# Kernel tuning notes

Measured on AMD Instinct MI355X. Metric: run time of the kernel, lower is better.

The kernel has to match this reference:

```python
import jax, jax.numpy as jnp
import numpy as np

B, A, H, W, N = 16, 9, 64, 64, 40


def setup_inputs() -> dict:
    key = jax.random.key(0)
    k1, k2, k3, k4, k5, k6 = jax.random.split(key, 6)
    # Anchor shapes (w, h) in pixel units, 9 anchors (3 scales x 3 aspect ratios)
    scales = jnp.array([32.0, 64.0, 128.0], dtype=jnp.float32)
    ratios = jnp.array([0.5, 1.0, 2.0], dtype=jnp.float32)
    ws = (scales[:, None] * jnp.sqrt(ratios)[None, :]).reshape(-1)  # (9,)
    hs = (scales[:, None] / jnp.sqrt(ratios)[None, :]).reshape(-1)
    anc = jnp.stack([ws, hs], axis=-1)  # (A, 2)
    # Grid of cell centers for a 512x512 image with stride 8 -> 64x64 grid
    stride = 8.0
    xs = (jnp.arange(W, dtype=jnp.float32) + 0.5) * stride
    ys = (jnp.arange(H, dtype=jnp.float32) + 0.5) * stride
    gx, gy = jnp.meshgrid(xs, ys, indexing='xy')  # (H, W)
    grid = jnp.broadcast_to(jnp.stack([gx, gy], axis=-1)[None], (B, H, W, 2)).astype(jnp.float32)
    # Predicted offsets: tx, ty in (-0.5, 0.5); tw, th small
    txy = jax.random.uniform(k1, (B, A, H, W, 2), jnp.float32, -0.5, 0.5)
    twh = jax.random.normal(k2, (B, A, H, W, 2), jnp.float32) * 0.2
    offsets = jnp.concatenate([txy, twh], axis=-1)  # (B, A, H, W, 4)
    # Ground-truth boxes (x_tl, y_tl, x_br, y_br, class), well-formed
    img = 512.0
    x1 = jax.random.uniform(k3, (B, N), jnp.float32, 0.0, img - 64.0)
    y1 = jax.random.uniform(k4, (B, N), jnp.float32, 0.0, img - 64.0)
    bw = jax.random.uniform(k5, (B, N), jnp.float32, 8.0, 64.0)
    bh = jax.random.uniform(k6, (B, N), jnp.float32, 8.0, 64.0)
    cls = jnp.zeros((B, N), jnp.float32)
    bboxes = jnp.stack([x1, y1, x1 + bw, y1 + bh, cls], axis=-1)  # (B, N, 5)
    return {"anc": anc, "grid": grid, "offsets": offsets, "bboxes": bboxes}


def reference(anc, grid, offsets, bboxes):
    # --- GenerateAnchor: (B, A, H, W, 4) corner boxes centered on grid ---
    half = (anc * 0.5)[None, :, None, None, :]      # (1, A, 1, 1, 2)
    g = grid[:, None]                               # (B, 1, H, W, 2)
    anchors = jnp.concatenate([g - half, g + half], axis=-1)  # (B, A, H, W, 4)

    # --- GenerateProposal (YOLO): center-shift by txy, scale wh by exp(twh) ---
    cx = (anchors[..., 0] + anchors[..., 2]) * 0.5 + offsets[..., 0]
    cy = (anchors[..., 1] + anchors[..., 3]) * 0.5 + offsets[..., 1]
    pw = (anchors[..., 2] - anchors[..., 0]) * jnp.exp(offsets[..., 2])
    ph = (anchors[..., 3] - anchors[..., 1]) * jnp.exp(offsets[..., 3])
    proposals = jnp.stack([cx - pw * 0.5, cy - ph * 0.5,
                           cx + pw * 0.5, cy + ph * 0.5], axis=-1)  # (B, A, H, W, 4)

    # --- IoU: (B, A*H*W, N) via broadcasting (no explicit repeat) ---
    Bsz = proposals.shape[0]
    p = proposals.reshape(Bsz, -1, 1, 4)   # (B, AHW, 1, 4)
    bb = bboxes[:, None, :, :4]            # (B, 1, N, 4)
    x_tl = jnp.maximum(p[..., 0], bb[..., 0])
    y_tl = jnp.maximum(p[..., 1], bb[..., 1])
    x_br = jnp.minimum(p[..., 2], bb[..., 2])
    y_br = jnp.minimum(p[..., 3], bb[..., 3])
    inter = jnp.clip(x_br - x_tl, 0.0) * jnp.clip(y_br - y_tl, 0.0)
    area_p = (p[..., 2] - p[..., 0]) * (p[..., 3] - p[..., 1])
    area_b = (bb[..., 2] - bb[..., 0]) * (bb[..., 3] - bb[..., 1])
    iou_mat = inter / (area_p + area_b - inter)    # (B, AHW, N)
    return iou_mat
```

## Files before the change

### kernel.cpp

```cpp
#include <hip/hip_runtime.h>

#define BB 16
#define AA 9
#define HH 64
#define WW 64
#define NN 40

constexpr int PPB   = AA * HH * WW;
constexpr int BLOCK = 256;
constexpr int BLOCKS_PER_B = PPB / BLOCK;
constexpr int F4_PER_P     = NN / 4;

typedef float vfloat4 __attribute__((ext_vector_type(4)));

__global__ __launch_bounds__(BLOCK) void iou_kernel(
    const float* __restrict__ anc,
    const float* __restrict__ grid,
    const float* __restrict__ offsets,
    const float* __restrict__ bboxes,
    float* __restrict__ out)
{
    __shared__ float4 sbox[NN];
    __shared__ float4 sp4[BLOCK];

    const int tid = threadIdx.x;
    const int blk = blockIdx.x;
    const int b        = blk / BLOCKS_PER_B;
    const int blk_in_b = blk % BLOCKS_PER_B;

    if (tid < NN) {
        const float* bb = bboxes + (size_t)(b * NN + tid) * 5;
        sbox[tid] = make_float4(bb[0], bb[1], bb[2], bb[3]);
    }

    const int p_in_b = blk_in_b * BLOCK + tid;
    const int a  = p_in_b >> 12;
    const int hw = p_in_b & 4095;
    const int h  = hw >> 6;
    const int w  = hw & 63;

    const float hwid = anc[a * 2 + 0] * 0.5f;
    const float hhgt = anc[a * 2 + 1] * 0.5f;

    const float2 g   = *reinterpret_cast<const float2*>(grid + (size_t)((b * HH + h) * WW + w) * 2);
    const float4 off = *reinterpret_cast<const float4*>(offsets + (size_t)(b * PPB + p_in_b) * 4);

    const float ax1 = g.x - hwid, ax2 = g.x + hwid;
    const float ay1 = g.y - hhgt, ay2 = g.y + hhgt;
    const float cx = (ax1 + ax2) * 0.5f + off.x;
    const float cy = (ay1 + ay2) * 0.5f + off.y;
    const float pw = (ax2 - ax1) * __expf(off.z);
    const float ph = (ay2 - ay1) * __expf(off.w);
    sp4[tid] = make_float4(cx - pw * 0.5f, cy - ph * 0.5f,
                           cx + pw * 0.5f, cy + ph * 0.5f);

    __syncthreads();

    vfloat4* outf4 = reinterpret_cast<vfloat4*>(out) +
                     (size_t)(b * PPB + blk_in_b * BLOCK) * F4_PER_P;

    #pragma unroll
    for (int i = 0; i < F4_PER_P; ++i) {
        const unsigned f = (unsigned)(tid + i * BLOCK);
        const unsigned p = f / 10u;
        const int n0 = (int)(f - p * 10u) * 4;

        const float4 pb = sp4[p];
        const float ap  = (pb.z - pb.x) * (pb.w - pb.y);

        vfloat4 res;
        #pragma unroll
        for (int k = 0; k < 4; ++k) {
            const float4 bb4 = sbox[n0 + k];
            const float ab  = (bb4.z - bb4.x) * (bb4.w - bb4.y);
            const float xtl = fmaxf(pb.x, bb4.x);
            const float ytl = fmaxf(pb.y, bb4.y);
            const float xbr = fminf(pb.z, bb4.z);
            const float ybr = fminf(pb.w, bb4.w);
            const float iw = fmaxf(xbr - xtl, 0.0f);
            const float ih = fmaxf(ybr - ytl, 0.0f);
            const float inter = iw * ih;
            const float den = ap + ab - inter;
            res[k] = inter * __builtin_amdgcn_rcpf(den);
        }
        __builtin_nontemporal_store(res, outf4 + f);
    }
}

extern "C" void kernel_launch(void* const* d_in, const int* in_sizes, int n_in,
                              void* d_out, int out_size, void* d_ws, size_t ws_size,
                              hipStream_t stream) {
    const float* anc     = (const float*)d_in[0];
    const float* grid    = (const float*)d_in[1];
    const float* offsets = (const float*)d_in[2];
    const float* bboxes  = (const float*)d_in[3];
    float* out = (float*)d_out;

    const int nblocks = BB * BLOCKS_PER_B;
    iou_kernel<<<nblocks, BLOCK, 0, stream>>>(anc, grid, offsets, bboxes, out);
}
```

Before: 21.69 us.

## Process two tiles per block with double-buffered shared memory prefetch

```diff
diff --git a/kernel.cpp b/kernel.cpp
--- a/kernel.cpp
+++ b/kernel.cpp
@@ -8,8 +8,11 @@
 
 constexpr int PPB   = AA * HH * WW;
 constexpr int BLOCK = 256;
-constexpr int BLOCKS_PER_B = PPB / BLOCK;
-constexpr int F4_PER_P     = NN / 4;
+constexpr int TPB   = PPB / BLOCK;
+constexpr int TILES = BB * TPB;
+constexpr int TILES_PER_BLOCK = 2;
+constexpr int NBLOCKS = TILES / TILES_PER_BLOCK;
+constexpr int F4_PER_P = NN / 4;
 
 typedef float vfloat4 __attribute__((ext_vector_type(4)));
 
@@ -20,71 +23,88 @@
     const float* __restrict__ bboxes,
     float* __restrict__ out)
 {
-    __shared__ float4 sbox[NN];
-    __shared__ float4 sp4[BLOCK];
+    __shared__ float4 sbox[2][NN];
+    __shared__ float4 sp4[2][BLOCK];
 
     const int tid = threadIdx.x;
-    const int blk = blockIdx.x;
-    const int b        = blk / BLOCKS_PER_B;
-    const int blk_in_b = blk % BLOCKS_PER_B;
 
-    if (tid < NN) {
-        const float* bb = bboxes + (size_t)(b * NN + tid) * 5;
-        sbox[tid] = make_float4(bb[0], bb[1], bb[2], bb[3]);
-    }
+    float2 g;  float4 off;  float hwid, hhgt;  float4 box;
 
-    const int p_in_b = blk_in_b * BLOCK + tid;
-    const int a  = p_in_b >> 12;
-    const int hw = p_in_b & 4095;
-    const int h  = hw >> 6;
-    const int w  = hw & 63;
+    auto load_tile = [&](int t) {
+        const int b  = t / TPB;
+        const int tb = t - b * TPB;
+        const int p  = tb * BLOCK + tid;
+        const int a  = p >> 12;
+        const int hw = p & 4095;
+        const int h  = hw >> 6;
+        const int w  = hw & 63;
+        hwid = anc[a * 2 + 0] * 0.5f;
+        hhgt = anc[a * 2 + 1] * 0.5f;
+        g   = *reinterpret_cast<const float2*>(grid + (size_t)((b * HH + h) * WW + w) * 2);
+        off = *reinterpret_cast<const float4*>(offsets + ((size_t)b * PPB + p) * 4);
+        if (tid < NN) {
+            const float* bb = bboxes + (size_t)(b * NN + tid) * 5;
+            box = make_float4(bb[0], bb[1], bb[2], bb[3]);
+        }
+    };
 
-    const float hwid = anc[a * 2 + 0] * 0.5f;
-    const float hhgt = anc[a * 2 + 1] * 0.5f;
+    auto decode_tile = [&](int buf) {
+        const float ax1 = g.x - hwid, ax2 = g.x + hwid;
+        const float ay1 = g.y - hhgt, ay2 = g.y + hhgt;
+        const float cx = (ax1 + ax2) * 0.5f + off.x;
+        const float cy = (ay1 + ay2) * 0.5f + off.y;
+        const float pw = (ax2 - ax1) * __expf(off.z);
+        const float ph = (ay2 - ay1) * __expf(off.w);
+        sp4[buf][tid] = make_float4(cx - pw * 0.5f, cy - ph * 0.5f,
+                                    cx + pw * 0.5f, cy + ph * 0.5f);
+        if (tid < NN) sbox[buf][tid] = box;
+    };
 
-    const float2 g   = *reinterpret_cast<const float2*>(grid + (size_t)((b * HH + h) * WW + w) * 2);
-    const float4 off = *reinterpret_cast<const float4*>(offsets + (size_t)(b * PPB + p_in_b) * 4);
+    auto store_tile = [&](int t, int buf) {
+        const int b  = t / TPB;
+        const int tb = t - b * TPB;
+        vfloat4* outf4 = reinterpret_cast<vfloat4*>(out) +
+                         ((size_t)b * PPB + (size_t)tb * BLOCK) * F4_PER_P;
+        #pragma unroll
+        for (int i = 0; i < F4_PER_P; ++i) {
+            const unsigned f = (unsigned)(tid + i * BLOCK);
+            const unsigned p = f / 10u;
+            const int n0 = (int)(f - p * 10u) * 4;
 
-    const float ax1 = g.x - hwid, ax2 = g.x + hwid;
-    const float ay1 = g.y - hhgt, ay2 = g.y + hhgt;
-    const float cx = (ax1 + ax2) * 0.5f + off.x;
-    const float cy = (ay1 + ay2) * 0.5f + off.y;
-    const float pw = (ax2 - ax1) * __expf(off.z);
-    const float ph = (ay2 - ay1) * __expf(off.w);
-    sp4[tid] = make_float4(cx - pw * 0.5f, cy - ph * 0.5f,
-                           cx + pw * 0.5f, cy + ph * 0.5f);
+            const float4 pb = sp4[buf][p];
+            const float ap  = (pb.z - pb.x) * (pb.w - pb.y);
 
+            vfloat4 res;
+            #pragma unroll
+            for (int k = 0; k < 4; ++k) {
+                const float4 bb4 = sbox[buf][n0 + k];
+                const float ab  = (bb4.z - bb4.x) * (bb4.w - bb4.y);
+                const float xtl = fmaxf(pb.x, bb4.x);
+                const float ytl = fmaxf(pb.y, bb4.y);
+                const float xbr = fminf(pb.z, bb4.z);
+                const float ybr = fminf(pb.w, bb4.w);
+                const float iw = fmaxf(xbr - xtl, 0.0f);
+                const float ih = fmaxf(ybr - ytl, 0.0f);
+                const float inter = iw * ih;
+                const float den = ap + ab - inter;
+                res[k] = inter * __builtin_amdgcn_rcpf(den);
+            }
+            __builtin_nontemporal_store(res, outf4 + f);
+        }
+    };
+
+    const int t0 = blockIdx.x * TILES_PER_BLOCK;
+
+    load_tile(t0);
+    decode_tile(0);
     __syncthreads();
 
-    vfloat4* outf4 = reinterpret_cast<vfloat4*>(out) +
-                     (size_t)(b * PPB + blk_in_b * BLOCK) * F4_PER_P;
+    load_tile(t0 + 1);
+    store_tile(t0, 0);
 
-    #pragma unroll
-    for (int i = 0; i < F4_PER_P; ++i) {
-        const unsigned f = (unsigned)(tid + i * BLOCK);
-        const unsigned p = f / 10u;
-        const int n0 = (int)(f - p * 10u) * 4;
-
-        const float4 pb = sp4[p];
-        const float ap  = (pb.z - pb.x) * (pb.w - pb.y);
-
-        vfloat4 res;
-        #pragma unroll
-        for (int k = 0; k < 4; ++k) {
-            const float4 bb4 = sbox[n0 + k];
-            const float ab  = (bb4.z - bb4.x) * (bb4.w - bb4.y);
-            const float xtl = fmaxf(pb.x, bb4.x);
-            const float ytl = fmaxf(pb.y, bb4.y);
-            const float xbr = fminf(pb.z, bb4.z);
-            const float ybr = fminf(pb.w, bb4.w);
-            const float iw = fmaxf(xbr - xtl, 0.0f);
-            const float ih = fmaxf(ybr - ytl, 0.0f);
-            const float inter = iw * ih;
-            const float den = ap + ab - inter;
-            res[k] = inter * __builtin_amdgcn_rcpf(den);
-        }
-        __builtin_nontemporal_store(res, outf4 + f);
-    }
+    decode_tile(1);
+    __syncthreads();
+    store_tile(t0 + 1, 1);
 }
 
 extern "C" void kernel_launch(void* const* d_in, const int* in_sizes, int n_in,
@@ -96,6 +116,5 @@
     const float* bboxes  = (const float*)d_in[3];
     float* out = (float*)d_out;
 
-    const int nblocks = BB * BLOCKS_PER_B;
-    iou_kernel<<<nblocks, BLOCK, 0, stream>>>(anc, grid, offsets, bboxes, out);
+    iou_kernel<<<NBLOCKS, BLOCK, 0, stream>>>(anc, grid, offsets, bboxes, out);
 }
```

New measurement: 25.18 us. 16.1% more time.
